# Optimization experiments

Hardware: AMD Instinct MI355X
Metric: run time of the kernel (lower is better)

## Reference

```python
import jax, jax.numpy as jnp
import numpy as np

NHEAD = 8
NEG_INF = -1e8

U, B, D = 2048, 4, 512
R, S, M = 64, 64, 64
Q = R + U + S
KV = M + R + U


def setup_inputs() -> dict:
    key = jax.random.key(0)
    ks = jax.random.split(key, 12)
    sd = 1.0 / np.sqrt(D)
    inp = {
        "utterance": jax.random.normal(ks[0], (U, B, D), jnp.float32),
        "lengths": jax.random.randint(ks[1], (B,), U // 2, U + 1),
        "right_context": jax.random.normal(ks[2], (R, B, D), jnp.float32),
        "summary": jax.random.normal(ks[3], (S, B, D), jnp.float32),
        "memory": jax.random.normal(ks[4], (M, B, D), jnp.float32),
        "attention_mask": jax.random.uniform(ks[5], (Q, KV)) < 0.3,
        "w_q": jax.random.normal(ks[6], (D, D), jnp.float32) * sd,
        "b_q": jax.random.normal(ks[7], (D,), jnp.float32) * 0.01,
        "w_kv": jax.random.normal(ks[8], (D, 2 * D), jnp.float32) * sd,
        "b_kv": jax.random.normal(ks[9], (2 * D,), jnp.float32) * 0.01,
        "w_out": jax.random.normal(ks[10], (D, D), jnp.float32) * sd,
        "b_out": jax.random.normal(ks[11], (D,), jnp.float32) * 0.01,
    }
    return inp


def reference(utterance, lengths, right_context, summary, memory,
              attention_mask, w_q, b_q, w_kv, b_kv, w_out, b_out):
    u_len, bsz, d = utterance.shape
    s_len = summary.shape[0]
    dh = d // NHEAD
    scaling = dh ** (-0.5)

    # Q = R + U + S ; KV = M + R + U
    q_in = jnp.concatenate([right_context, utterance, summary], axis=0)
    kv_in = jnp.concatenate([memory, right_context, utterance], axis=0)

    query = q_in @ w_q + b_q                      # (Q, B, D)
    kv = kv_in @ w_kv + b_kv                      # (KV, B, 2D)
    key_t, value = kv[..., :d], kv[..., d:]

    q_len, kv_len = query.shape[0], key_t.shape[0]
    q = query.reshape(q_len, bsz, NHEAD, dh)
    k = key_t.reshape(kv_len, bsz, NHEAD, dh)
    v = value.reshape(kv_len, bsz, NHEAD, dh)

    # (B, H, Q, KV) attention logits, computed in fp32 (matches .float())
    logits = jnp.einsum("qbhd,kbhd->bhqk", (q * scaling).astype(jnp.float32),
                        k.astype(jnp.float32))
    logits = jnp.where(attention_mask[None, None], NEG_INF, logits)

    if bsz > 1:
        # padding mask over keys: position j padded if j >= KV - U + lengths[b]
        pad = jnp.arange(kv_len)[None, :] >= (kv_len - u_len + lengths)[:, None]
        logits = jnp.where(pad[:, None, None, :], NEG_INF, logits)

    probs = jax.nn.softmax(logits, axis=-1).astype(q.dtype)
    attn = jnp.einsum("bhqk,kbhd->qbhd", probs, v).reshape(q_len, bsz, d)
    outputs = attn @ w_out + b_out                # (Q, B, D)

    out_rcu = outputs[: q_len - s_len]            # (R+U, B, D)
    out_mem = jnp.clip(outputs[q_len - s_len:], -10.0, 10.0)  # tanh_on_mem=False
    return out_rcu, out_mem[:-1]                  # memory output has length S-1
```

## Files before the change

### kernel.cpp

```cpp
#include <hip/hip_runtime.h>
#include <cmath>
#include <cstddef>

#define QLEN 2176
#define NROWS 8704
#define NEG_INF_V -100000000.0f
#define NMASK ((size_t)QLEN * (size_t)QLEN)
#define NBITW (4 * QLEN * 68)

typedef __attribute__((ext_vector_type(8))) short short8;
typedef __attribute__((ext_vector_type(4))) float f32x4;
typedef __attribute__((ext_vector_type(16))) float f32x16;
typedef unsigned short ushort_t;

#define MFMA16(A, B, C) __builtin_amdgcn_mfma_f32_16x16x32_bf16(A, B, C, 0, 0, 0)
#define MFMA32(A, B, C) __builtin_amdgcn_mfma_f32_32x32x16_bf16(A, B, C, 0, 0, 0)

#if __has_builtin(__builtin_amdgcn_exp2f)
#define EXP2(x) __builtin_amdgcn_exp2f(x)
#else
#define EXP2(x) __expf((x) * 0.6931471805599453f)
#endif

__device__ __forceinline__ ushort_t f2bf(float f) {
    unsigned int u = __builtin_bit_cast(unsigned int, f);
    u += 0x7FFFu + ((u >> 16) & 1u);
    return (ushort_t)(u >> 16);
}

__device__ __forceinline__ unsigned int cvtpk_bf16(float lo, float hi) {
    unsigned int r;
    asm volatile("v_cvt_pk_bf16_f32 %0, %1, %2" : "=v"(r) : "v"(lo), "v"(hi));
    return r;
}

__device__ __forceinline__ void gload16(const void* g, void* l) {
    __builtin_amdgcn_global_load_lds(
        (const __attribute__((address_space(1))) void*)g,
        (__attribute__((address_space(3))) void*)l, 16, 0, 0);
}

__global__ __launch_bounds__(256) void detect_mask_kernel(
    const unsigned int* __restrict__ m, int* __restrict__ flag)
{
    __shared__ unsigned int r123, r01, r23;
    if (threadIdx.x == 0) { r123 = 0; r01 = 0; r23 = 0; }
    __syncthreads();
    unsigned int a123 = 0, a01 = 0, a23 = 0;
    #pragma unroll
    for (int i = 0; i < 16; ++i) {
        unsigned int w = m[threadIdx.x * 16 + i];
        a123 |= (w & 0xFFFFFF00u);
        a01  |= (w & 0x0000FFFFu);
        a23  |= (w & 0xFFFF0000u);
    }
    if (a123) atomicOr(&r123, 1u);
    if (a01)  atomicOr(&r01, 1u);
    if (a23)  atomicOr(&r23, 1u);
    __syncthreads();
    if (threadIdx.x == 0) {
        int f;
        if (!r123)            f = 0;
        else if (!r01 && r23) f = 2;
        else                  f = 1;
        *flag = f;
    }
}

__global__ __launch_bounds__(256) void canon_bits_kernel(
    const void* __restrict__ mraw, const int* __restrict__ flag,
    const int* __restrict__ lengths, unsigned int* __restrict__ bits)
{
    int idx = blockIdx.x * 256 + threadIdx.x;
    if (idx >= NBITW) return;
    int b = idx / (QLEN * 68);
    int rem = idx - b * (QLEN * 68);
    int q = rem / 68, w = rem - q * 68;
    int kv0 = w * 32;
    int f = *flag;
    unsigned int out = 0;
    if (f == 1) {
        const uint4* p = (const uint4*)((const unsigned char*)mraw + (size_t)q * QLEN + kv0);
        uint4 va = p[0], vb = p[1];
        unsigned int ws2[8] = {va.x, va.y, va.z, va.w, vb.x, vb.y, vb.z, vb.w};
        #pragma unroll
        for (int ww = 0; ww < 8; ++ww) {
            unsigned int x = ws2[ww];
            #pragma unroll
            for (int j = 0; j < 4; ++j)
                out |= ((x >> (8 * j)) & 0xFFu) ? (1u << (ww * 4 + j)) : 0u;
        }
    } else {
        const uint4* p = (const uint4*)((const unsigned int*)mraw + (size_t)q * QLEN + kv0);
        #pragma unroll
        for (int g2 = 0; g2 < 8; ++g2) {
            uint4 v = p[g2];
            out |= (v.x ? 1u : 0u) << (g2 * 4);
            out |= (v.y ? 2u : 0u) << (g2 * 4);
            out |= (v.z ? 4u : 0u) << (g2 * 4);
            out |= (v.w ? 8u : 0u) << (g2 * 4);
        }
    }
    int n = (128 + lengths[b]) - kv0;
    unsigned int pm = (n <= 0) ? 0xFFFFFFFFu : (n >= 32 ? 0u : (0xFFFFFFFFu << n));
    bits[idx] = out | pm;
}

__global__ __launch_bounds__(256) void conv_concat(
    const float* __restrict__ s0, const float* __restrict__ s1, const float* __restrict__ s2,
    int b0, int b1, ushort_t* __restrict__ dst)
{
    int c = blockIdx.x * 256 + threadIdx.x;
    int row = c >> 6, ch = c & 63;
    if (row >= NROWS) return;
    const float* src;
    if (row < b0)      src = s0 + (size_t)row * 512;
    else if (row < b1) src = s1 + (size_t)(row - b0) * 512;
    else               src = s2 + (size_t)(row - b1) * 512;
    float4 v0 = *(const float4*)(src + ch * 8);
    float4 v1 = *(const float4*)(src + ch * 8 + 4);
    short8 o;
    o[0] = (short)f2bf(v0.x); o[1] = (short)f2bf(v0.y);
    o[2] = (short)f2bf(v0.z); o[3] = (short)f2bf(v0.w);
    o[4] = (short)f2bf(v1.x); o[5] = (short)f2bf(v1.y);
    o[6] = (short)f2bf(v1.z); o[7] = (short)f2bf(v1.w);
    *(short8*)(dst + (size_t)row * 512 + ch * 8) = o;
}

__global__ __launch_bounds__(256) void transpose_w_all(
    const float* __restrict__ w_q, const float* __restrict__ w_kv,
    const float* __restrict__ w_out,
    ushort_t* __restrict__ wtq, ushort_t* __restrict__ wtkv, ushort_t* __restrict__ wtout)
{
    __shared__ float t[32][33];
    int bx = blockIdx.x;
    const float* W; ushort_t* Wt; int N, nb;
    if (bx < 16)      { W = w_q;   Wt = wtq;   N = 512;  nb = bx; }
    else if (bx < 48) { W = w_kv;  Wt = wtkv;  N = 1024; nb = bx - 16; }
    else              { W = w_out; Wt = wtout; N = 512;  nb = bx - 48; }
    int n0 = nb * 32, k0 = blockIdx.y * 32;
    int tx = threadIdx.x & 31, ty = threadIdx.x >> 5;
    #pragma unroll
    for (int i = 0; i < 4; ++i)
        t[ty + 8 * i][tx] = W[(size_t)(k0 + ty + 8 * i) * N + n0 + tx];
    __syncthreads();
    #pragma unroll
    for (int i = 0; i < 4; ++i)
        Wt[(size_t)(n0 + ty + 8 * i) * 512 + k0 + tx] = f2bf(t[tx][ty + 8 * i]);
}

template<int MODE, int ASRC>
__global__ __launch_bounds__(256) void gemm_mfma(
    const ushort_t* __restrict__ A,
    const float* __restrict__ s0, const float* __restrict__ s1, const float* __restrict__ s2,
    int b0, int b1,
    const ushort_t* __restrict__ Bt,
    const float* __restrict__ bias, float scale,
    ushort_t* __restrict__ dst0, ushort_t* __restrict__ dst1,
    float* __restrict__ dstf)
{
    __shared__ __align__(16) ushort_t As[128][32];
    __shared__ __align__(16) ushort_t Bs[128][32];
    const int tid = threadIdx.x;
    const int wid = tid >> 6, lane = tid & 63, lr = lane & 15, lg = lane >> 4;
    const int wm = wid >> 1, wn = wid & 1;
    const int bm = blockIdx.x, bn = blockIdx.y;

    f32x4 acc[4][4] = {};

    for (int k0 = 0; k0 < 512; k0 += 32) {
        __syncthreads();
        #pragma unroll
        for (int i = 0; i < 2; ++i) {
            const int q = wid * 128 + 64 * i + lane;
            const int row = q >> 2, pc = q & 3;
            const int sc = pc ^ (row & 3);
            if (ASRC == 0) {
                gload16(A + (size_t)(bm * 128 + row) * 512 + k0 + sc * 8,
                        (ushort_t*)As + (size_t)(wid * 128 + 64 * i) * 8);
            } else {
                int gr = bm * 128 + row;
                const float* src;
                if (gr < b0)      src = s0 + (size_t)gr * 512;
                else if (gr < b1) src = s1 + (size_t)(gr - b0) * 512;
                else              src = s2 + (size_t)(gr - b1) * 512;
                float4 v0 = *(const float4*)(src + k0 + sc * 8);
                float4 v1 = *(const float4*)(src + k0 + sc * 8 + 4);
                short8 o;
                o[0] = (short)f2bf(v0.x); o[1] = (short)f2bf(v0.y);
                o[2] = (short)f2bf(v0.z); o[3] = (short)f2bf(v0.w);
                o[4] = (short)f2bf(v1.x); o[5] = (short)f2bf(v1.y);
                o[6] = (short)f2bf(v1.z); o[7] = (short)f2bf(v1.w);
                *(short8*)&As[row][pc * 8] = o;
            }
            gload16(Bt + (size_t)(bn * 128 + row) * 512 + k0 + sc * 8,
                    (ushort_t*)Bs + (size_t)(wid * 128 + 64 * i) * 8);
        }
        __syncthreads();
        short8 af[4], bf[4];
        #pragma unroll
        for (int i = 0; i < 4; ++i) {
            const int ra = wm * 64 + i * 16 + lr;
            const int rb = wn * 64 + i * 16 + lr;
            af[i] = *(const short8*)&As[ra][(lg ^ (ra & 3)) * 8];
            bf[i] = *(const short8*)&Bs[rb][(lg ^ (rb & 3)) * 8];
        }
        #pragma unroll
        for (int i = 0; i < 4; ++i)
            #pragma unroll
            for (int j = 0; j < 4; ++j)
                acc[i][j] = MFMA16(af[i], bf[j], acc[i][j]);
    }

    #pragma unroll
    for (int i = 0; i < 4; ++i) {
        #pragma unroll
        for (int j = 0; j < 4; ++j) {
            int gc = bn * 128 + wn * 64 + j * 16 + lr;
            float bv = bias[gc];
            #pragma unroll
            for (int r = 0; r < 4; ++r) {
                int gr = bm * 128 + wm * 64 + i * 16 + lg * 4 + r;
                float v = (acc[i][j][r] + bv) * scale;
                if (MODE == 0) {
                    int cc = gc;
                    ushort_t* d = dst0;
                    if (cc >= 512) { cc -= 512; d = dst1; }
                    int pos = gr >> 2, bb = gr & 3;
                    d[(((size_t)bb * 8 + (cc >> 6)) * QLEN + pos) * 64 + (cc & 63)] = f2bf(v);
                } else {
                    int q = gr >> 2, bb = gr & 3;
                    if (q < 2112) {
                        dstf[(size_t)gr * 512 + gc] = v;
                    } else if (q < 2175) {
                        float cv = fminf(10.0f, fmaxf(-10.0f, v));
                        dstf[(size_t)2112 * 4 * 512 + ((size_t)(q - 2112) * 4 + bb) * 512 + gc] = cv;
                    }
                }
            }
        }
    }
}

__global__ __launch_bounds__(256) void attn_mfma32(
    const ushort_t* __restrict__ Qa, const ushort_t* __restrict__ Ka,
    const ushort_t* __restrict__ Va,
    const unsigned int* __restrict__ mbits,
    ushort_t* __restrict__ attnb)
{
    __shared__ __align__(16) ushort_t Ks[64][72];
    __shared__ __align__(16) ushort_t Vt[64][72];

    const int swz = (blockIdx.x & 7) * 68 + (blockIdx.x >> 3);
    const int qt = swz % 17, bh = swz / 17;
    const int b = bh >> 3, h = bh & 7;
    const int tid = threadIdx.x;
    const int w = tid >> 6, lane = tid & 63;
    const int ql = lane & 31, hi = lane >> 5;
    const size_t hb = (size_t)bh * QLEN * 64;
    const int qrow = qt * 128 + w * 32 + ql;

    short8 bq[4];
    #pragma unroll
    for (int m = 0; m < 4; ++m)
        bq[m] = *(const short8*)(Qa + hb + (size_t)qrow * 64 + m * 16 + hi * 8);

    const unsigned int* mrow = mbits + ((size_t)b * QLEN + qrow) * 68;

    f32x16 oacc[2] = {};
    float lsum16[16];
    #pragma unroll
    for (int r = 0; r < 16; ++r) lsum16[r] = 0.0f;

    for (int kt = 0; kt < 34; ++kt) {
        const int k0 = kt * 64;
        __syncthreads();
        #pragma unroll
        for (int p2 = 0; p2 < 2; ++p2) {
            int c = p2 * 256 + tid;
            int row = c >> 3, ch = c & 7;
            *(short8*)&Ks[row][ch * 8] =
                *(const short8*)(Ka + hb + (size_t)(k0 + row) * 64 + ch * 8);
        }
        #pragma unroll
        for (int p2 = 0; p2 < 2; ++p2) {
            int c = p2 * 256 + tid;
            int kv = c & 63, ch = c >> 6;
            short8 v = *(const short8*)(Va + hb + (size_t)(k0 + kv) * 64 + ch * 8);
            #pragma unroll
            for (int i = 0; i < 8; ++i) Vt[ch * 8 + i][kv] = (ushort_t)v[i];
        }
        __syncthreads();

        f32x16 st[2] = {};
        __builtin_amdgcn_s_setprio(1);
        #pragma unroll
        for (int t = 0; t < 2; ++t)
            #pragma unroll
            for (int m = 0; m < 4; ++m) {
                short8 ak = *(const short8*)&Ks[t * 32 + ql][m * 16 + hi * 8];
                st[t] = MFMA32(ak, bq[m], st[t]);
            }
        __builtin_amdgcn_s_setprio(0);

        unsigned int wm0 = mrow[kt * 2]     >> (hi * 4);
        unsigned int wm1 = mrow[kt * 2 + 1] >> (hi * 4);
        float p[2][16];
        #pragma unroll
        for (int t = 0; t < 2; ++t) {
            unsigned int wt = t ? wm1 : wm0;
            #pragma unroll
            for (int r = 0; r < 16; ++r) {
                const int rl = (r & 3) + 8 * (r >> 2);
                float x = ((wt >> rl) & 1u) ? NEG_INF_V : st[t][r];
                p[t][r] = EXP2(x);
            }
        }
        #pragma unroll
        for (int r = 0; r < 16; ++r) lsum16[r] += p[0][r] + p[1][r];

        unsigned int bw[4][4];
        #pragma unroll
        for (int c = 0; c < 4; ++c) {
            const int t0 = c >> 1, s0 = (2 * c) & 3, s1 = s0 + 1;
            unsigned int A = cvtpk_bf16(p[t0][4 * s0 + 0], p[t0][4 * s0 + 1]);
            unsigned int B = cvtpk_bf16(p[t0][4 * s1 + 0], p[t0][4 * s1 + 1]);
            unsigned int C = cvtpk_bf16(p[t0][4 * s0 + 2], p[t0][4 * s0 + 3]);
            unsigned int D = cvtpk_bf16(p[t0][4 * s1 + 2], p[t0][4 * s1 + 3]);
            asm volatile("v_permlane32_swap_b32 %0, %1" : "+v"(A), "+v"(B));
            asm volatile("v_permlane32_swap_b32 %0, %1" : "+v"(C), "+v"(D));
            bw[c][0] = A; bw[c][1] = C; bw[c][2] = B; bw[c][3] = D;
        }

        __builtin_amdgcn_s_setprio(1);
        #pragma unroll
        for (int c = 0; c < 4; ++c) {
            uint4 t4; t4.x = bw[c][0]; t4.y = bw[c][1]; t4.z = bw[c][2]; t4.w = bw[c][3];
            short8 bp = __builtin_bit_cast(short8, t4);
            #pragma unroll
            for (int dt = 0; dt < 2; ++dt) {
                short8 av = *(const short8*)&Vt[dt * 32 + ql][c * 16 + hi * 8];
                oacc[dt] = MFMA32(av, bp, oacc[dt]);
            }
        }
        __builtin_amdgcn_s_setprio(0);
    }

    #pragma unroll
    for (int s = 8; s; s >>= 1)
        #pragma unroll
        for (int r = 0; r < s; ++r) lsum16[r] += lsum16[r + s];
    float lsum = lsum16[0] + __shfl_xor(lsum16[0], 32);

    float inv = 1.0f / lsum;
    #pragma unroll
    for (int dt = 0; dt < 2; ++dt)
        #pragma unroll
        for (int s = 0; s < 4; ++s) {
            unsigned int lo = (unsigned int)f2bf(oacc[dt][4 * s + 0] * inv)
                            | ((unsigned int)f2bf(oacc[dt][4 * s + 1] * inv) << 16);
            unsigned int hi2 = (unsigned int)f2bf(oacc[dt][4 * s + 2] * inv)
                             | ((unsigned int)f2bf(oacc[dt][4 * s + 3] * inv) << 16);
            uint2 pk; pk.x = lo; pk.y = hi2;
            *(uint2*)(attnb + ((size_t)qrow * 4 + b) * 512 + h * 64 + dt * 32 + 8 * s + 4 * hi) = pk;
        }
}

extern "C" void kernel_launch(void* const* d_in, const int* in_sizes, int n_in,
                              void* d_out, int out_size, void* d_ws, size_t ws_size,
                              hipStream_t stream) {
    const float* utterance     = (const float*)d_in[0];
    const int*   lengths       = (const int*)d_in[1];
    const float* right_context = (const float*)d_in[2];
    const float* summary       = (const float*)d_in[3];
    const float* memory        = (const float*)d_in[4];
    const void*  mask_raw      = d_in[5];
    const float* w_q   = (const float*)d_in[6];
    const float* b_q   = (const float*)d_in[7];
    const float* w_kv  = (const float*)d_in[8];
    const float* b_kv  = (const float*)d_in[9];
    const float* w_out = (const float*)d_in[10];
    const float* b_out = (const float*)d_in[11];
    float* out = (float*)d_out;

    char* ws = (char*)d_ws;
    const size_t SZ = (size_t)NROWS * 512 * 2;
    ushort_t* kvin   = (ushort_t*)(ws);
    ushort_t* q_attn = (ushort_t*)(ws + SZ);
    ushort_t* k_attn = (ushort_t*)(ws + 2 * SZ);
    ushort_t* v_attn = (ushort_t*)(ws + 3 * SZ);
    ushort_t* attnb  = (ushort_t*)(ws + 4 * SZ);
    ushort_t* wtq    = (ushort_t*)(ws + 5 * SZ);
    ushort_t* wtkv   = wtq + (size_t)512 * 512;
    ushort_t* wtout  = wtkv + (size_t)1024 * 512;
    unsigned int* mbits = (unsigned int*)(wtout + (size_t)512 * 512);
    int* maskflag = (int*)(mbits + NBITW);

    detect_mask_kernel<<<1, 256, 0, stream>>>((const unsigned int*)mask_raw, maskflag);
    canon_bits_kernel<<<(NBITW + 255) / 256, 256, 0, stream>>>(mask_raw, maskflag, lengths, mbits);

    conv_concat<<<2176, 256, 0, stream>>>(memory, right_context, utterance, 256, 512, kvin);

    transpose_w_all<<<dim3(64, 16), 256, 0, stream>>>(w_q, w_kv, w_out, wtq, wtkv, wtout);

    const float qscale = 0.125f * 1.4426950408889634f;
    gemm_mfma<0, 1><<<dim3(68, 4), 256, 0, stream>>>(
        nullptr, right_context, utterance, summary, 256, 8448,
        wtq, b_q, qscale, q_attn, q_attn, nullptr);
    gemm_mfma<0, 0><<<dim3(68, 8), 256, 0, stream>>>(
        kvin, nullptr, nullptr, nullptr, 0, 0,
        wtkv, b_kv, 1.0f, k_attn, v_attn, nullptr);

    attn_mfma32<<<544, 256, 0, stream>>>(q_attn, k_attn, v_attn, mbits, attnb);

    gemm_mfma<1, 0><<<dim3(68, 4), 256, 0, stream>>>(
        attnb, nullptr, nullptr, nullptr, 0, 0,
        wtout, b_out, 1.0f, nullptr, nullptr, out);
}
```

Baseline: 176.1 us.

## Merge prep kernels and Q/KV projections into single launches with LDS-staged stores

The separate mask-detection, mask canonicalisation, concat-convert and weight-transpose kernels become one prep launch that branches on block index. Each block now recomputes the mask format flag with wave ballots, so the one-block detect kernel and its dependency are gone. The Q and KV projection GEMMs are merged into one grid, and their epilogue stages results through LDS so each head row goes out as 16-byte vector stores instead of scattered 2-byte writes. Together this cuts launch count and serialization, at the cost of redundant flag reads in every canon block and extra LDS traffic in the epilogue.

```diff
diff --git a/kernel.cpp b/kernel.cpp
--- a/kernel.cpp
+++ b/kernel.cpp
@@ -5,8 +5,11 @@
 #define QLEN 2176
 #define NROWS 8704
 #define NEG_INF_V -100000000.0f
-#define NMASK ((size_t)QLEN * (size_t)QLEN)
 #define NBITW (4 * QLEN * 68)
+
+#define CANON_BLKS 2312
+#define CONV_BLKS  2176
+#define TRANS_BLKS 1024
 
 typedef __attribute__((ext_vector_type(8))) short short8;
 typedef __attribute__((ext_vector_type(4))) float f32x4;
@@ -40,131 +43,117 @@
         (__attribute__((address_space(3))) void*)l, 16, 0, 0);
 }
 
-__global__ __launch_bounds__(256) void detect_mask_kernel(
-    const unsigned int* __restrict__ m, int* __restrict__ flag)
-{
-    __shared__ unsigned int r123, r01, r23;
-    if (threadIdx.x == 0) { r123 = 0; r01 = 0; r23 = 0; }
-    __syncthreads();
-    unsigned int a123 = 0, a01 = 0, a23 = 0;
-    #pragma unroll
-    for (int i = 0; i < 16; ++i) {
-        unsigned int w = m[threadIdx.x * 16 + i];
-        a123 |= (w & 0xFFFFFF00u);
-        a01  |= (w & 0x0000FFFFu);
-        a23  |= (w & 0xFFFF0000u);
-    }
-    if (a123) atomicOr(&r123, 1u);
-    if (a01)  atomicOr(&r01, 1u);
-    if (a23)  atomicOr(&r23, 1u);
-    __syncthreads();
-    if (threadIdx.x == 0) {
-        int f;
-        if (!r123)            f = 0;
-        else if (!r01 && r23) f = 2;
-        else                  f = 1;
-        *flag = f;
-    }
-}
-
-__global__ __launch_bounds__(256) void canon_bits_kernel(
-    const void* __restrict__ mraw, const int* __restrict__ flag,
-    const int* __restrict__ lengths, unsigned int* __restrict__ bits)
-{
-    int idx = blockIdx.x * 256 + threadIdx.x;
-    if (idx >= NBITW) return;
-    int b = idx / (QLEN * 68);
-    int rem = idx - b * (QLEN * 68);
-    int q = rem / 68, w = rem - q * 68;
-    int kv0 = w * 32;
-    int f = *flag;
-    unsigned int out = 0;
-    if (f == 1) {
-        const uint4* p = (const uint4*)((const unsigned char*)mraw + (size_t)q * QLEN + kv0);
-        uint4 va = p[0], vb = p[1];
-        unsigned int ws2[8] = {va.x, va.y, va.z, va.w, vb.x, vb.y, vb.z, vb.w};
-        #pragma unroll
-        for (int ww = 0; ww < 8; ++ww) {
-            unsigned int x = ws2[ww];
-            #pragma unroll
-            for (int j = 0; j < 4; ++j)
-                out |= ((x >> (8 * j)) & 0xFFu) ? (1u << (ww * 4 + j)) : 0u;
-        }
-    } else {
-        const uint4* p = (const uint4*)((const unsigned int*)mraw + (size_t)q * QLEN + kv0);
-        #pragma unroll
-        for (int g2 = 0; g2 < 8; ++g2) {
-            uint4 v = p[g2];
-            out |= (v.x ? 1u : 0u) << (g2 * 4);
-            out |= (v.y ? 2u : 0u) << (g2 * 4);
-            out |= (v.z ? 4u : 0u) << (g2 * 4);
-            out |= (v.w ? 8u : 0u) << (g2 * 4);
-        }
-    }
-    int n = (128 + lengths[b]) - kv0;
-    unsigned int pm = (n <= 0) ? 0xFFFFFFFFu : (n >= 32 ? 0u : (0xFFFFFFFFu << n));
-    bits[idx] = out | pm;
-}
-
-__global__ __launch_bounds__(256) void conv_concat(
-    const float* __restrict__ s0, const float* __restrict__ s1, const float* __restrict__ s2,
-    int b0, int b1, ushort_t* __restrict__ dst)
-{
-    int c = blockIdx.x * 256 + threadIdx.x;
-    int row = c >> 6, ch = c & 63;
-    if (row >= NROWS) return;
-    const float* src;
-    if (row < b0)      src = s0 + (size_t)row * 512;
-    else if (row < b1) src = s1 + (size_t)(row - b0) * 512;
-    else               src = s2 + (size_t)(row - b1) * 512;
-    float4 v0 = *(const float4*)(src + ch * 8);
-    float4 v1 = *(const float4*)(src + ch * 8 + 4);
-    short8 o;
-    o[0] = (short)f2bf(v0.x); o[1] = (short)f2bf(v0.y);
-    o[2] = (short)f2bf(v0.z); o[3] = (short)f2bf(v0.w);
-    o[4] = (short)f2bf(v1.x); o[5] = (short)f2bf(v1.y);
-    o[6] = (short)f2bf(v1.z); o[7] = (short)f2bf(v1.w);
-    *(short8*)(dst + (size_t)row * 512 + ch * 8) = o;
-}
-
-__global__ __launch_bounds__(256) void transpose_w_all(
+__global__ __launch_bounds__(256) void prep_kernel(
+    const void* __restrict__ mraw, const int* __restrict__ lengths,
+    unsigned int* __restrict__ bits,
+    const float* __restrict__ memory, const float* __restrict__ right_context,
+    const float* __restrict__ utterance, ushort_t* __restrict__ kvin,
     const float* __restrict__ w_q, const float* __restrict__ w_kv,
     const float* __restrict__ w_out,
     ushort_t* __restrict__ wtq, ushort_t* __restrict__ wtkv, ushort_t* __restrict__ wtout)
 {
     __shared__ float t[32][33];
-    int bx = blockIdx.x;
-    const float* W; ushort_t* Wt; int N, nb;
-    if (bx < 16)      { W = w_q;   Wt = wtq;   N = 512;  nb = bx; }
-    else if (bx < 48) { W = w_kv;  Wt = wtkv;  N = 1024; nb = bx - 16; }
-    else              { W = w_out; Wt = wtout; N = 512;  nb = bx - 48; }
-    int n0 = nb * 32, k0 = blockIdx.y * 32;
-    int tx = threadIdx.x & 31, ty = threadIdx.x >> 5;
-    #pragma unroll
-    for (int i = 0; i < 4; ++i)
-        t[ty + 8 * i][tx] = W[(size_t)(k0 + ty + 8 * i) * N + n0 + tx];
-    __syncthreads();
-    #pragma unroll
-    for (int i = 0; i < 4; ++i)
-        Wt[(size_t)(n0 + ty + 8 * i) * 512 + k0 + tx] = f2bf(t[tx][ty + 8 * i]);
-}
-
-template<int MODE, int ASRC>
-__global__ __launch_bounds__(256) void gemm_mfma(
-    const ushort_t* __restrict__ A,
+    const int bx = blockIdx.x;
+    if (bx < CANON_BLKS) {
+        const unsigned int* mw = (const unsigned int*)mraw;
+        unsigned int a123 = 0, a01 = 0, a23 = 0;
+        #pragma unroll
+        for (int i = 0; i < 16; ++i) {
+            unsigned int wv = mw[(threadIdx.x & 63) * 16 + i];
+            a123 |= wv & 0xFFFFFF00u;
+            a01  |= wv & 0x0000FFFFu;
+            a23  |= wv & 0xFFFF0000u;
+        }
+        int f;
+        if (__ballot(a123 != 0) == 0)                                 f = 0;
+        else if (__ballot(a01 != 0) == 0 && __ballot(a23 != 0) != 0)  f = 2;
+        else                                                          f = 1;
+
+        int idx = bx * 256 + threadIdx.x;
+        if (idx >= NBITW) return;
+        int b = idx / (QLEN * 68);
+        int rem = idx - b * (QLEN * 68);
+        int q = rem / 68, w = rem - q * 68;
+        int kv0 = w * 32;
+        unsigned int out = 0;
+        if (f == 1) {
+            const uint4* p = (const uint4*)((const unsigned char*)mraw + (size_t)q * QLEN + kv0);
+            uint4 va = p[0], vb = p[1];
+            unsigned int ws2[8] = {va.x, va.y, va.z, va.w, vb.x, vb.y, vb.z, vb.w};
+            #pragma unroll
+            for (int ww = 0; ww < 8; ++ww) {
+                unsigned int x = ws2[ww];
+                #pragma unroll
+                for (int j = 0; j < 4; ++j)
+                    out |= ((x >> (8 * j)) & 0xFFu) ? (1u << (ww * 4 + j)) : 0u;
+            }
+        } else {
+            const uint4* p = (const uint4*)((const unsigned int*)mraw + (size_t)q * QLEN + kv0);
+            #pragma unroll
+            for (int g2 = 0; g2 < 8; ++g2) {
+                uint4 v = p[g2];
+                out |= (v.x ? 1u : 0u) << (g2 * 4);
+                out |= (v.y ? 2u : 0u) << (g2 * 4);
+                out |= (v.z ? 4u : 0u) << (g2 * 4);
+                out |= (v.w ? 8u : 0u) << (g2 * 4);
+            }
+        }
+        int n = (128 + lengths[b]) - kv0;
+        unsigned int pm = (n <= 0) ? 0xFFFFFFFFu : (n >= 32 ? 0u : (0xFFFFFFFFu << n));
+        bits[idx] = out | pm;
+    } else if (bx < CANON_BLKS + CONV_BLKS) {
+        int c = (bx - CANON_BLKS) * 256 + threadIdx.x;
+        int row = c >> 6, ch = c & 63;
+        if (row >= NROWS) return;
+        const float* src;
+        if (row < 256)      src = memory + (size_t)row * 512;
+        else if (row < 512) src = right_context + (size_t)(row - 256) * 512;
+        else                src = utterance + (size_t)(row - 512) * 512;
+        float4 v0 = *(const float4*)(src + ch * 8);
+        float4 v1 = *(const float4*)(src + ch * 8 + 4);
+        short8 o;
+        o[0] = (short)f2bf(v0.x); o[1] = (short)f2bf(v0.y);
+        o[2] = (short)f2bf(v0.z); o[3] = (short)f2bf(v0.w);
+        o[4] = (short)f2bf(v1.x); o[5] = (short)f2bf(v1.y);
+        o[6] = (short)f2bf(v1.z); o[7] = (short)f2bf(v1.w);
+        *(short8*)(kvin + (size_t)row * 512 + ch * 8) = o;
+    } else {
+        int idx = bx - (CANON_BLKS + CONV_BLKS);
+        int xb = idx & 63, yb = idx >> 6;
+        const float* W; ushort_t* Wt; int N, nb;
+        if (xb < 16)      { W = w_q;   Wt = wtq;   N = 512;  nb = xb; }
+        else if (xb < 48) { W = w_kv;  Wt = wtkv;  N = 1024; nb = xb - 16; }
+        else              { W = w_out; Wt = wtout; N = 512;  nb = xb - 48; }
+        int n0 = nb * 32, k0 = yb * 32;
+        int tx = threadIdx.x & 31, ty = threadIdx.x >> 5;
+        #pragma unroll
+        for (int i = 0; i < 4; ++i)
+            t[ty + 8 * i][tx] = W[(size_t)(k0 + ty + 8 * i) * N + n0 + tx];
+        __syncthreads();
+        #pragma unroll
+        for (int i = 0; i < 4; ++i)
+            Wt[(size_t)(n0 + ty + 8 * i) * 512 + k0 + tx] = f2bf(t[tx][ty + 8 * i]);
+    }
+}
+
+__global__ __launch_bounds__(256) void proj_mfma(
     const float* __restrict__ s0, const float* __restrict__ s1, const float* __restrict__ s2,
-    int b0, int b1,
-    const ushort_t* __restrict__ Bt,
-    const float* __restrict__ bias, float scale,
-    ushort_t* __restrict__ dst0, ushort_t* __restrict__ dst1,
-    float* __restrict__ dstf)
+    const ushort_t* __restrict__ kvin,
+    const ushort_t* __restrict__ wtq, const ushort_t* __restrict__ wtkv,
+    const float* __restrict__ b_q, const float* __restrict__ b_kv, float qscale,
+    ushort_t* __restrict__ q_attn, ushort_t* __restrict__ k_attn, ushort_t* __restrict__ v_attn)
 {
     __shared__ __align__(16) ushort_t As[128][32];
     __shared__ __align__(16) ushort_t Bs[128][32];
     const int tid = threadIdx.x;
     const int wid = tid >> 6, lane = tid & 63, lr = lane & 15, lg = lane >> 4;
     const int wm = wid >> 1, wn = wid & 1;
-    const int bm = blockIdx.x, bn = blockIdx.y;
+    const int bm = blockIdx.x;
+    const bool isQ = (blockIdx.y < 4);
+    const int bn = isQ ? blockIdx.y : blockIdx.y - 4;
+    const ushort_t* Bt = isQ ? wtq : wtkv;
+    const float* bias  = isQ ? b_q : b_kv;
+    const float scale  = isQ ? qscale : 1.0f;
 
     f32x4 acc[4][4] = {};
 
@@ -175,15 +164,12 @@
             const int q = wid * 128 + 64 * i + lane;
             const int row = q >> 2, pc = q & 3;
             const int sc = pc ^ (row & 3);
-            if (ASRC == 0) {
-                gload16(A + (size_t)(bm * 128 + row) * 512 + k0 + sc * 8,
-                        (ushort_t*)As + (size_t)(wid * 128 + 64 * i) * 8);
-            } else {
+            if (isQ) {
                 int gr = bm * 128 + row;
                 const float* src;
-                if (gr < b0)      src = s0 + (size_t)gr * 512;
-                else if (gr < b1) src = s1 + (size_t)(gr - b0) * 512;
-                else              src = s2 + (size_t)(gr - b1) * 512;
+                if (gr < 256)       src = s0 + (size_t)gr * 512;
+                else if (gr < 8448) src = s1 + (size_t)(gr - 256) * 512;
+                else                src = s2 + (size_t)(gr - 8448) * 512;
                 float4 v0 = *(const float4*)(src + k0 + sc * 8);
                 float4 v1 = *(const float4*)(src + k0 + sc * 8 + 4);
                 short8 o;
@@ -192,6 +178,9 @@
                 o[4] = (short)f2bf(v1.x); o[5] = (short)f2bf(v1.y);
                 o[6] = (short)f2bf(v1.z); o[7] = (short)f2bf(v1.w);
                 *(short8*)&As[row][pc * 8] = o;
+            } else {
+                gload16(kvin + (size_t)(bm * 128 + row) * 512 + k0 + sc * 8,
+                        (ushort_t*)As + (size_t)(wid * 128 + 64 * i) * 8);
             }
             gload16(Bt + (size_t)(bn * 128 + row) * 512 + k0 + sc * 8,
                     (ushort_t*)Bs + (size_t)(wid * 128 + 64 * i) * 8);
@@ -212,6 +201,85 @@
                 acc[i][j] = MFMA16(af[i], bf[j], acc[i][j]);
     }
 
+    __syncthreads();
+    const int gcb = bn * 128 + wn * 64;
+    ushort_t* dbase; int ccb;
+    if (isQ)              { dbase = q_attn; ccb = gcb >> 6; }
+    else if (gcb >= 512)  { dbase = v_attn; ccb = (gcb - 512) >> 6; }
+    else                  { dbase = k_attn; ccb = gcb >> 6; }
+    ushort_t* Wr = ((wid & 2) ? &Bs[0][0] : &As[0][0]) + (wid & 1) * 2048;
+    #pragma unroll
+    for (int h = 0; h < 2; ++h) {
+        #pragma unroll
+        for (int ii = 0; ii < 2; ++ii) {
+            const int i = h * 2 + ii;
+            #pragma unroll
+            for (int j = 0; j < 4; ++j) {
+                const int colb = j * 16 + lr;
+                const float bv = bias[gcb + colb];
+                #pragma unroll
+                for (int r = 0; r < 4; ++r) {
+                    const int rowl = ii * 16 + lg * 4 + r;
+                    const int phys = (colb >> 3) ^ (rowl & 7);
+                    Wr[rowl * 64 + phys * 8 + (colb & 7)] =
+                        f2bf((acc[i][j][r] + bv) * scale);
+                }
+            }
+        }
+        const int rl2 = lane >> 1;
+        const int gr = bm * 128 + wm * 64 + h * 32 + rl2;
+        const int q2 = gr >> 2, b2 = gr & 3;
+        ushort_t* drow = dbase + (((size_t)b2 * 8 + ccb) * QLEN + q2) * 64;
+        #pragma unroll
+        for (int k = 0; k < 4; ++k) {
+            const int ch2 = (lane & 1) * 4 + k;
+            const int phys = ch2 ^ (rl2 & 7);
+            *(short8*)(drow + ch2 * 8) = *(const short8*)&Wr[rl2 * 64 + phys * 8];
+        }
+    }
+}
+
+__global__ __launch_bounds__(256) void gemm_out(
+    const ushort_t* __restrict__ A, const ushort_t* __restrict__ Bt,
+    const float* __restrict__ bias, float* __restrict__ dstf)
+{
+    __shared__ __align__(16) ushort_t As[128][32];
+    __shared__ __align__(16) ushort_t Bs[128][32];
+    const int tid = threadIdx.x;
+    const int wid = tid >> 6, lane = tid & 63, lr = lane & 15, lg = lane >> 4;
+    const int wm = wid >> 1, wn = wid & 1;
+    const int bm = blockIdx.x, bn = blockIdx.y;
+
+    f32x4 acc[4][4] = {};
+
+    for (int k0 = 0; k0 < 512; k0 += 32) {
+        __syncthreads();
+        #pragma unroll
+        for (int i = 0; i < 2; ++i) {
+            const int q = wid * 128 + 64 * i + lane;
+            const int row = q >> 2, pc = q & 3;
+            const int sc = pc ^ (row & 3);
+            gload16(A + (size_t)(bm * 128 + row) * 512 + k0 + sc * 8,
+                    (ushort_t*)As + (size_t)(wid * 128 + 64 * i) * 8);
+            gload16(Bt + (size_t)(bn * 128 + row) * 512 + k0 + sc * 8,
+                    (ushort_t*)Bs + (size_t)(wid * 128 + 64 * i) * 8);
+        }
+        __syncthreads();
+        short8 af[4], bf[4];
+        #pragma unroll
+        for (int i = 0; i < 4; ++i) {
+            const int ra = wm * 64 + i * 16 + lr;
+            const int rb = wn * 64 + i * 16 + lr;
+            af[i] = *(const short8*)&As[ra][(lg ^ (ra & 3)) * 8];
+            bf[i] = *(const short8*)&Bs[rb][(lg ^ (rb & 3)) * 8];
+        }
+        #pragma unroll
+        for (int i = 0; i < 4; ++i)
+            #pragma unroll
+            for (int j = 0; j < 4; ++j)
+                acc[i][j] = MFMA16(af[i], bf[j], acc[i][j]);
+    }
+
     #pragma unroll
     for (int i = 0; i < 4; ++i) {
         #pragma unroll
@@ -221,21 +289,13 @@
             #pragma unroll
             for (int r = 0; r < 4; ++r) {
                 int gr = bm * 128 + wm * 64 + i * 16 + lg * 4 + r;
-                float v = (acc[i][j][r] + bv) * scale;
-                if (MODE == 0) {
-                    int cc = gc;
-                    ushort_t* d = dst0;
-                    if (cc >= 512) { cc -= 512; d = dst1; }
-                    int pos = gr >> 2, bb = gr & 3;
-                    d[(((size_t)bb * 8 + (cc >> 6)) * QLEN + pos) * 64 + (cc & 63)] = f2bf(v);
-                } else {
-                    int q = gr >> 2, bb = gr & 3;
-                    if (q < 2112) {
-                        dstf[(size_t)gr * 512 + gc] = v;
-                    } else if (q < 2175) {
-                        float cv = fminf(10.0f, fmaxf(-10.0f, v));
-                        dstf[(size_t)2112 * 4 * 512 + ((size_t)(q - 2112) * 4 + bb) * 512 + gc] = cv;
-                    }
+                float v = acc[i][j][r] + bv;
+                int q = gr >> 2, bb = gr & 3;
+                if (q < 2112) {
+                    dstf[(size_t)gr * 512 + gc] = v;
+                } else if (q < 2175) {
+                    float cv = fminf(10.0f, fmaxf(-10.0f, v));
+                    dstf[(size_t)2112 * 4 * 512 + ((size_t)(q - 2112) * 4 + bb) * 512 + gc] = cv;
                 }
             }
         }
@@ -394,26 +454,19 @@
     ushort_t* wtkv   = wtq + (size_t)512 * 512;
     ushort_t* wtout  = wtkv + (size_t)1024 * 512;
     unsigned int* mbits = (unsigned int*)(wtout + (size_t)512 * 512);
-    int* maskflag = (int*)(mbits + NBITW);
-
-    detect_mask_kernel<<<1, 256, 0, stream>>>((const unsigned int*)mask_raw, maskflag);
-    canon_bits_kernel<<<(NBITW + 255) / 256, 256, 0, stream>>>(mask_raw, maskflag, lengths, mbits);
-
-    conv_concat<<<2176, 256, 0, stream>>>(memory, right_context, utterance, 256, 512, kvin);
-
-    transpose_w_all<<<dim3(64, 16), 256, 0, stream>>>(w_q, w_kv, w_out, wtq, wtkv, wtout);
+
+    prep_kernel<<<CANON_BLKS + CONV_BLKS + TRANS_BLKS, 256, 0, stream>>>(
+        mask_raw, lengths, mbits,
+        memory, right_context, utterance, kvin,
+        w_q, w_kv, w_out, wtq, wtkv, wtout);
 
     const float qscale = 0.125f * 1.4426950408889634f;
-    gemm_mfma<0, 1><<<dim3(68, 4), 256, 0, stream>>>(
-        nullptr, right_context, utterance, summary, 256, 8448,
-        wtq, b_q, qscale, q_attn, q_attn, nullptr);
-    gemm_mfma<0, 0><<<dim3(68, 8), 256, 0, stream>>>(
-        kvin, nullptr, nullptr, nullptr, 0, 0,
-        wtkv, b_kv, 1.0f, k_attn, v_attn, nullptr);
+    proj_mfma<<<dim3(68, 12), 256, 0, stream>>>(
+        right_context, utterance, summary, kvin,
+        wtq, wtkv, b_q, b_kv, qscale,
+        q_attn, k_attn, v_attn);
 
     attn_mfma32<<<544, 256, 0, stream>>>(q_attn, k_attn, v_attn, mbits, attnb);
 
-    gemm_mfma<1, 0><<<dim3(68, 4), 256, 0, stream>>>(
-        attnb, nullptr, nullptr, nullptr, 0, 0,
-        wtout, b_out, 1.0f, nullptr, nullptr, out);
-}
+    gemm_out<<<dim3(68, 4), 256, 0, stream>>>(attnb, wtout, b_out, out);
+}
```

Result: faster. 162.8 us (-7.6%).
